# Kernel tuning notes

Measured on AMD Instinct MI355X. Metric: run time of the kernel, lower is better.

Reference implementation:

```python
import jax, jax.numpy as jnp
import numpy as np

EMBED_DIM = 1024
Q_DIM = 512
KV_DIM = 512
NUM_HEADS = 16
HEAD_DIM = EMBED_DIM // NUM_HEADS
EPS = 1e-5


def setup_inputs() -> dict:
    key = jax.random.key(0)
    ks = jax.random.split(key, 13)
    B, N1, N2 = 2, 2048, 2048
    s_q = 1.0 / np.sqrt(Q_DIM)
    s_kv = 1.0 / np.sqrt(KV_DIM)
    s_e = 1.0 / np.sqrt(EMBED_DIM)
    return {
        "query": jax.random.normal(ks[0], (B, N1, Q_DIM), jnp.float32),
        "key": jax.random.normal(ks[1], (B, N2, KV_DIM), jnp.float32),
        "value": jax.random.normal(ks[2], (B, N2, KV_DIM), jnp.float32),
        "Wq": jax.random.uniform(ks[3], (Q_DIM, EMBED_DIM), jnp.float32, -s_q, s_q),
        "bq": jax.random.uniform(ks[4], (EMBED_DIM,), jnp.float32, -s_q, s_q),
        "Wk": jax.random.uniform(ks[5], (KV_DIM, EMBED_DIM), jnp.float32, -s_kv, s_kv),
        "bk": jax.random.uniform(ks[6], (EMBED_DIM,), jnp.float32, -s_kv, s_kv),
        "Wv": jax.random.uniform(ks[7], (KV_DIM, EMBED_DIM), jnp.float32, -s_kv, s_kv),
        "bv": jax.random.uniform(ks[8], (EMBED_DIM,), jnp.float32, -s_kv, s_kv),
        "Wo": jax.random.uniform(ks[9], (EMBED_DIM, EMBED_DIM), jnp.float32, -s_e, s_e),
        "bo": jax.random.uniform(ks[10], (EMBED_DIM,), jnp.float32, -s_e, s_e),
        "gamma": jnp.ones((EMBED_DIM,), jnp.float32),
        "beta": jnp.zeros((EMBED_DIM,), jnp.float32),
    }


def reference(query, key, value, Wq, bq, Wk, bk, Wv, bv, Wo, bo, gamma, beta):
    B, N1, _ = query.shape
    _, N2, _ = key.shape
    scale = HEAD_DIM ** (-0.5)
    # projections -> [B, H, N, D]
    Q = (query @ Wq + bq).reshape(B, N1, NUM_HEADS, HEAD_DIM).transpose(0, 2, 1, 3)
    K = (key @ Wk + bk).reshape(B, N2, NUM_HEADS, HEAD_DIM).transpose(0, 2, 1, 3)
    V = (value @ Wv + bv).reshape(B, N2, NUM_HEADS, HEAD_DIM).transpose(0, 2, 1, 3)
    # full score matrix [B, H, N1, N2] (matches original eager attention)
    att = jnp.einsum("bhqd,bhkd->bhqk", Q, K) * scale
    att = jax.nn.softmax(att, axis=-1)
    # dropout is identity in eval mode
    out = jnp.einsum("bhqk,bhkd->bhqd", att, V)  # [B, H, N1, D]
    out = out.transpose(0, 2, 1, 3).reshape(B, N1, EMBED_DIM)
    out = out @ Wo + bo
    # LayerNorm
    mu = out.mean(-1, keepdims=True)
    var = ((out - mu) ** 2).mean(-1, keepdims=True)
    return (out - mu) * jax.lax.rsqrt(var + EPS) * gamma + beta
```

## Files before the change

kernel.cpp:

```cpp
#include <hip/hip_runtime.h>

typedef __bf16 bf16x8 __attribute__((ext_vector_type(8)));
typedef __bf16 bf16x4 __attribute__((ext_vector_type(4)));
typedef __bf16 bf16x2 __attribute__((ext_vector_type(2)));
typedef float f32x4 __attribute__((ext_vector_type(4)));
typedef unsigned short u16;
typedef unsigned int u32;

__device__ __forceinline__ f32x4 mfma16(bf16x8 a, bf16x8 b, f32x4 c) {
  return __builtin_amdgcn_mfma_f32_16x16x32_bf16(a, b, c, 0, 0, 0);
}

__device__ __forceinline__ void gload_lds16(const void* g, void* l) {
  __builtin_amdgcn_global_load_lds(
      (const __attribute__((address_space(1))) void*)g,
      (__attribute__((address_space(3))) void*)l, 16, 0, 0);
}

__device__ __forceinline__ void swap32(u32& a, u32& b) {
  asm volatile("v_permlane32_swap_b32 %0, %1" : "+v"(a), "+v"(b));
}
__device__ __forceinline__ void swap16(u32& a, u32& b) {
  asm volatile("v_permlane16_swap_b32 %0, %1" : "+v"(a), "+v"(b));
}

__device__ __forceinline__ u32 pkbf(float a, float b) {
  union { bf16x2 h; u32 w; } u;
  u.h[0] = (__bf16)a;
  u.h[1] = (__bf16)b;
  return u.w;
}

__global__ __launch_bounds__(256) void prep(const float4* __restrict__ qi,
                                            const float4* __restrict__ ki,
                                            const float4* __restrict__ vi,
                                            bf16x4* __restrict__ oq,
                                            bf16x4* __restrict__ ok,
                                            bf16x4* __restrict__ ov,
                                            const float* __restrict__ W0,
                                            const float* __restrict__ W1,
                                            const float* __restrict__ W2,
                                            const float* __restrict__ W3,
                                            u16* __restrict__ T0, u16* __restrict__ T1,
                                            u16* __restrict__ T2, u16* __restrict__ T3,
                                            int n4) {
  const int z = blockIdx.y;
  const int tid = threadIdx.x;
  if (z < 3) {
    int i = blockIdx.x * 256 + tid;
    if (i >= n4) return;
    const float4* in = z == 0 ? qi : z == 1 ? ki : vi;
    bf16x4* out = z == 0 ? oq : z == 1 ? ok : ov;
    float4 v = in[i];
    bf16x4 o;
    o[0] = (__bf16)v.x; o[1] = (__bf16)v.y; o[2] = (__bf16)v.z; o[3] = (__bf16)v.w;
    out[i] = o;
  } else {
    const int zz = z - 3;
    const int K = (zz == 3) ? 1024 : 512;
    const int nb = (K / 32) * 32;
    if (blockIdx.x >= nb) return;
    const float* W = zz == 0 ? W0 : zz == 1 ? W1 : zz == 2 ? W2 : W3;
    u16* Wt = zz == 0 ? T0 : zz == 1 ? T1 : zz == 2 ? T2 : T3;
    __shared__ float t[32][33];
    const int tx = tid & 31, ty = tid >> 5;
    const int n0 = (blockIdx.x & 31) * 32, k0 = (blockIdx.x >> 5) * 32;
#pragma unroll
    for (int i = 0; i < 4; ++i)
      t[ty + i * 8][tx] = W[(size_t)(k0 + ty + i * 8) * 1024 + n0 + tx];
    __syncthreads();
#pragma unroll
    for (int i = 0; i < 4; ++i)
      ((__bf16*)Wt)[(size_t)(n0 + ty + i * 8) * K + k0 + tx] = (__bf16)t[tx][ty + i * 8];
  }
}

template <int MODE, int DBUF>
__device__ __forceinline__ void gemm_body(const u16* __restrict__ A,
                                          const u16* __restrict__ Bt,
                                          const float* __restrict__ bias,
                                          void* __restrict__ Cout,
                                          int M, int N, int K, float scl) {
  constexpr int NB = DBUF ? 2 : 1;
  __shared__ __align__(16) u16 lA[NB][128 * 64];
  __shared__ __align__(16) u16 lB[NB][128 * 64];
  const int tid = threadIdx.x;
  const int w = tid >> 6, l = tid & 63;
  const int li = l & 15, lg = l >> 4;
  const int wm = w & 1, wn = w >> 1;
  const int bm = blockIdx.x * 128, bn = blockIdx.y * 128;

  f32x4 acc[4][4] = {};
  const int nk = K >> 6;

  auto stage = [&](int kt, int bufi) {
    const int k0 = kt << 6;
#pragma unroll
    for (int i = 0; i < 4; ++i) {
      const int c0 = (i * 4 + w) * 64;
      const int f = c0 + l;
      const int r = f >> 3, cs = (f & 7) ^ (r & 7);
      gload_lds16(A + (size_t)(bm + r) * K + k0 + cs * 8, &lA[bufi][c0 * 8]);
      gload_lds16(Bt + (size_t)(bn + r) * K + k0 + cs * 8, &lB[bufi][c0 * 8]);
    }
  };

  int cur = 0;
  if (DBUF) {
    stage(0, 0);
    __syncthreads();
  }

  for (int kt = 0; kt < nk; ++kt) {
    if (DBUF) {
      if (kt + 1 < nk) stage(kt + 1, cur ^ 1);
    } else {
      stage(kt, 0);
      __syncthreads();
    }
    bf16x8 af[4][2], bfr[4][2];
#pragma unroll
    for (int m = 0; m < 4; ++m) {
      const int row = wm * 64 + m * 16 + li;
#pragma unroll
      for (int kk = 0; kk < 2; ++kk) {
        const int kc = (lg + kk * 4) ^ (row & 7);
        af[m][kk] = *(const bf16x8*)&lA[cur][row * 64 + kc * 8];
      }
    }
#pragma unroll
    for (int n = 0; n < 4; ++n) {
      const int row = wn * 64 + n * 16 + li;
#pragma unroll
      for (int kk = 0; kk < 2; ++kk) {
        const int kc = (lg + kk * 4) ^ (row & 7);
        bfr[n][kk] = *(const bf16x8*)&lB[cur][row * 64 + kc * 8];
      }
    }
#pragma unroll
    for (int m = 0; m < 4; ++m)
#pragma unroll
      for (int n = 0; n < 4; ++n) {
        acc[m][n] = mfma16(af[m][0], bfr[n][0], acc[m][n]);
        acc[m][n] = mfma16(af[m][1], bfr[n][1], acc[m][n]);
      }
    __syncthreads();
    if (DBUF) cur ^= 1;
  }

#pragma unroll
  for (int m = 0; m < 4; ++m) {
    const int row0 = bm + wm * 64 + m * 16 + lg * 4;
#pragma unroll
    for (int n = 0; n < 4; ++n) {
      const int col = bn + wn * 64 + n * 16 + li;
      const float bv = bias[col];
      if (MODE == 2) {
        const int bq = row0 >> 11, kv = row0 & 2047;
        bf16x4 pk;
#pragma unroll
        for (int r = 0; r < 4; ++r) pk[r] = (__bf16)((acc[m][n][r] + bv) * scl);
        *(bf16x4*)&((u16*)Cout)[((size_t)(bq * 1024 + col)) * 2048 + kv] = pk;
      } else {
#pragma unroll
        for (int r = 0; r < 4; ++r) {
          float v = (acc[m][n][r] + bv) * scl;
          ((__bf16*)Cout)[(size_t)(row0 + r) * N + col] = (__bf16)v;
        }
      }
    }
  }
}

__global__ __launch_bounds__(256) void gemm_qkv(const u16* __restrict__ xq,
                                                const u16* __restrict__ xk,
                                                const u16* __restrict__ xv,
                                                const u16* __restrict__ wqt,
                                                const u16* __restrict__ wkt,
                                                const u16* __restrict__ wvt,
                                                const float* __restrict__ bq,
                                                const float* __restrict__ bk,
                                                const float* __restrict__ bv,
                                                u16* __restrict__ Qb, u16* __restrict__ Kb,
                                                u16* __restrict__ Vt, float qscale) {
  const int z = blockIdx.z;
  if (z == 0) {
    gemm_body<0, 0>(xq, wqt, bq, Qb, 4096, 1024, 512, qscale);
  } else if (z == 1) {
    gemm_body<0, 0>(xk, wkt, bk, Kb, 4096, 1024, 512, 1.0f);
  } else {
    gemm_body<2, 0>(xv, wvt, bv, Vt, 4096, 1024, 512, 1.0f);
  }
}

__global__ __launch_bounds__(256) void gemm_o(const u16* __restrict__ A,
                                              const u16* __restrict__ Bt,
                                              const float* __restrict__ bias,
                                              u16* __restrict__ C) {
  gemm_body<0, 1>(A, Bt, bias, C, 4096, 1024, 1024, 1.0f);
}

__global__ __launch_bounds__(512) void attn64(const u16* __restrict__ Qb,
                                              const u16* __restrict__ Kb,
                                              const u16* __restrict__ Vt,
                                              u16* __restrict__ Opart,
                                              float* __restrict__ Lpart,
                                              int N1, int N2) {
  const int tid = threadIdx.x;
  const int w = tid >> 6, l = tid & 63;
  const int li = l & 15, lg = l >> 4;

  const int flat = blockIdx.x + 8 * (blockIdx.y + 16 * blockIdx.z);
  const int xcd = flat & 7, idx = flat >> 3;
  const int qb = idx & 7, rest = idx >> 3;
  const int h = 2 * xcd + (rest & 1);
  const int b = (rest >> 1) & 1;
  const int kvh = rest >> 2;
  const int q0 = qb * 256;

  __shared__ __align__(16) u16 lK[2][64 * 64];
  __shared__ __align__(16) u16 lV[2][64 * 64];

  bf16x8 qa[2][2];
#pragma unroll
  for (int s = 0; s < 2; ++s) {
    const size_t qoff = (size_t)(b * N1 + q0 + s * 128 + w * 16 + li) * 1024 + h * 64;
    qa[s][0] = *(const bf16x8*)&Qb[qoff + lg * 8];
    qa[s][1] = *(const bf16x8*)&Qb[qoff + 32 + lg * 8];
  }

  const u16* Kbase = Kb + (size_t)b * N2 * 1024 + h * 64;
  const u16* Vbase = Vt + (size_t)((b * 16 + h) * 64) * N2;

  const int sr = tid >> 3;
  const int sc = (tid & 7) ^ (sr & 7);

  f32x4 o[2][4] = {};
  float lsum0 = 0.f, lsum1 = 0.f;
  const int ca = lg ^ (li & 7), cb = (lg + 4) ^ (li & 7);

  const int t0 = kvh * 16;
  int cur = 0;
  gload_lds16(Kbase + (size_t)(t0 * 64 + sr) * 1024 + sc * 8, &lK[0][w * 512]);
  gload_lds16(Vbase + (size_t)sr * N2 + t0 * 64 + sc * 8, &lV[0][w * 512]);
  __syncthreads();

  for (int tt = 0; tt < 16; ++tt) {
    const int t = t0 + tt;
    if (tt + 1 < 16) {
      gload_lds16(Kbase + (size_t)((t + 1) * 64 + sr) * 1024 + sc * 8, &lK[cur ^ 1][w * 512]);
      gload_lds16(Vbase + (size_t)sr * N2 + (t + 1) * 64 + sc * 8, &lV[cur ^ 1][w * 512]);
    }
    const u16* K_ = lK[cur];
    const u16* V_ = lV[cur];

    float st0 = 0.f, st1 = 0.f;
    u32 u0[4][2], u1[4][2];
    __builtin_amdgcn_s_setprio(1);
#pragma unroll
    for (int n = 0; n < 4; ++n) {
      const int row = n * 16 + li;
      bf16x8 k0 = *(const bf16x8*)&K_[row * 64 + ca * 8];
      bf16x8 k1 = *(const bf16x8*)&K_[row * 64 + cb * 8];
      f32x4 a = {}, a2 = {};
      a = mfma16(k0, qa[0][0], a);
      a = mfma16(k1, qa[0][1], a);
      a2 = mfma16(k0, qa[1][0], a2);
      a2 = mfma16(k1, qa[1][1], a2);
      float p0 = __builtin_amdgcn_exp2f(a[0]);
      float p1 = __builtin_amdgcn_exp2f(a[1]);
      float p2 = __builtin_amdgcn_exp2f(a[2]);
      float p3 = __builtin_amdgcn_exp2f(a[3]);
      st0 += (p0 + p1) + (p2 + p3);
      u0[n][0] = pkbf(p0, p1);
      u0[n][1] = pkbf(p2, p3);
      float r0 = __builtin_amdgcn_exp2f(a2[0]);
      float r1 = __builtin_amdgcn_exp2f(a2[1]);
      float r2 = __builtin_amdgcn_exp2f(a2[2]);
      float r3 = __builtin_amdgcn_exp2f(a2[3]);
      st1 += (r0 + r1) + (r2 + r3);
      u1[n][0] = pkbf(r0, r1);
      u1[n][1] = pkbf(r2, r3);
    }
    __builtin_amdgcn_s_setprio(0);
    lsum0 += st0;
    lsum1 += st1;

#pragma unroll
    for (int c = 0; c < 2; ++c) {
      swap32(u0[0][c], u0[1][c]); swap32(u0[2][c], u0[3][c]);
      swap32(u1[0][c], u1[1][c]); swap32(u1[2][c], u1[3][c]);
    }
#pragma unroll
    for (int c = 0; c < 2; ++c) {
      swap16(u0[0][c], u0[1][c]); swap16(u0[2][c], u0[3][c]);
      swap16(u1[0][c], u1[1][c]); swap16(u1[2][c], u1[3][c]);
    }

    __builtin_amdgcn_s_setprio(1);
#pragma unroll
    for (int ks = 0; ks < 2; ++ks) {
      union { u32 w4[4]; bf16x8 v; } f0, f1;
      f0.w4[0] = u0[2 * ks][0]; f0.w4[1] = u0[2 * ks][1];
      f0.w4[2] = u0[2 * ks + 1][0]; f0.w4[3] = u0[2 * ks + 1][1];
      f1.w4[0] = u1[2 * ks][0]; f1.w4[1] = u1[2 * ks][1];
      f1.w4[2] = u1[2 * ks + 1][0]; f1.w4[3] = u1[2 * ks + 1][1];
#pragma unroll
      for (int dt = 0; dt < 4; ++dt) {
        const int row = dt * 16 + li;
        const int c = (lg + ks * 4) ^ (li & 7);
        const bf16x8 vf = *(const bf16x8*)&V_[row * 64 + c * 8];
        o[0][dt] = mfma16(vf, f0.v, o[0][dt]);
        o[1][dt] = mfma16(vf, f1.v, o[1][dt]);
      }
    }
    __builtin_amdgcn_s_setprio(0);
    __syncthreads();
    cur ^= 1;
  }

  lsum0 += __shfl_xor(lsum0, 16, 64);
  lsum0 += __shfl_xor(lsum0, 32, 64);
  lsum1 += __shfl_xor(lsum1, 16, 64);
  lsum1 += __shfl_xor(lsum1, 32, 64);

  u16* Op = Opart + (size_t)kvh * 4096 * 1024;
#pragma unroll
  for (int s = 0; s < 2; ++s) {
    const int qrow = b * N1 + q0 + s * 128 + w * 16 + li;
    const size_t orow = (size_t)qrow * 1024 + h * 64;
#pragma unroll
    for (int dt = 0; dt < 4; ++dt) {
      bf16x4 pk;
#pragma unroll
      for (int r = 0; r < 4; ++r) pk[r] = (__bf16)o[s][dt][r];
      *(bf16x4*)&Op[orow + dt * 16 + lg * 4] = pk;
    }
    if (lg == 0)
      Lpart[(size_t)kvh * 4096 * 16 + (size_t)qrow * 16 + h] = (s == 0 ? lsum0 : lsum1);
  }
}

__global__ __launch_bounds__(256) void combine(const u16* __restrict__ Opart,
                                               const float* __restrict__ Lpart,
                                               u16* __restrict__ ao) {
  const int row = blockIdx.x;
  const int tid = threadIdx.x;
  const int h = tid >> 4;
  const float l = Lpart[(size_t)row * 16 + h] + Lpart[4096 * 16 + (size_t)row * 16 + h];
  const float inv = 1.f / l;
  const size_t off = (size_t)row * 1024 + tid * 4;
  const bf16x4 a = *(const bf16x4*)&Opart[off];
  const bf16x4 b = *(const bf16x4*)&Opart[(size_t)4096 * 1024 + off];
  bf16x4 o;
#pragma unroll
  for (int j = 0; j < 4; ++j) o[j] = (__bf16)(((float)a[j] + (float)b[j]) * inv);
  *(bf16x4*)&ao[off] = o;
}

__global__ __launch_bounds__(256) void lnorm(const u16* __restrict__ X,
                                             const float* __restrict__ gamma,
                                             const float* __restrict__ beta,
                                             float* __restrict__ out) {
  const int row = blockIdx.x;
  const int tid = threadIdx.x;
  const bf16x4 xv = ((const bf16x4*)(X + (size_t)row * 1024))[tid];
  float4 v;
  v.x = (float)xv[0]; v.y = (float)xv[1]; v.z = (float)xv[2]; v.w = (float)xv[3];
  float s = v.x + v.y + v.z + v.w;
  float sq = v.x * v.x + v.y * v.y + v.z * v.z + v.w * v.w;
#pragma unroll
  for (int d = 1; d < 64; d <<= 1) {
    s += __shfl_xor(s, d, 64);
    sq += __shfl_xor(sq, d, 64);
  }
  __shared__ float red[8];
  const int w = tid >> 6, l = tid & 63;
  if (l == 0) { red[w] = s; red[4 + w] = sq; }
  __syncthreads();
  s = red[0] + red[1] + red[2] + red[3];
  sq = red[4] + red[5] + red[6] + red[7];
  const float mu = s * (1.f / 1024.f);
  const float var = sq * (1.f / 1024.f) - mu * mu;
  const float rstd = rsqrtf(var + 1e-5f);
  const float4 g = ((const float4*)gamma)[tid];
  const float4 bb = ((const float4*)beta)[tid];
  float4 o;
  o.x = (v.x - mu) * rstd * g.x + bb.x;
  o.y = (v.y - mu) * rstd * g.y + bb.y;
  o.z = (v.z - mu) * rstd * g.z + bb.z;
  o.w = (v.w - mu) * rstd * g.w + bb.w;
  ((float4*)(out + (size_t)row * 1024))[tid] = o;
}

extern "C" void kernel_launch(void* const* d_in, const int* in_sizes, int n_in,
                              void* d_out, int out_size, void* d_ws, size_t ws_size,
                              hipStream_t stream) {
  const float* query = (const float*)d_in[0];
  const float* key_ = (const float*)d_in[1];
  const float* value = (const float*)d_in[2];
  const float* Wq = (const float*)d_in[3];
  const float* bq = (const float*)d_in[4];
  const float* Wk = (const float*)d_in[5];
  const float* bk = (const float*)d_in[6];
  const float* Wv = (const float*)d_in[7];
  const float* bv = (const float*)d_in[8];
  const float* Wo = (const float*)d_in[9];
  const float* bo = (const float*)d_in[10];
  const float* gamma = (const float*)d_in[11];
  const float* beta = (const float*)d_in[12];

  constexpr int B = 2, N1 = 2048, N2 = 2048, E = 1024, QKD = 512;
  constexpr int M = B * N1;
  const float QSCALE = 0.125f * 1.4426950408889634f;

  char* p = (char*)d_ws;
  auto alloc = [&](size_t bytes) {
    char* r = p;
    p += (bytes + 255) & ~(size_t)255;
    return r;
  };
  u16* xq = (u16*)alloc((size_t)M * QKD * 2);
  u16* xk = (u16*)alloc((size_t)M * QKD * 2);
  u16* xv = (u16*)alloc((size_t)M * QKD * 2);
  u16* wqt = (u16*)alloc((size_t)E * QKD * 2);
  u16* wkt = (u16*)alloc((size_t)E * QKD * 2);
  u16* wvt = (u16*)alloc((size_t)E * QKD * 2);
  u16* wot = (u16*)alloc((size_t)E * E * 2);
  u16* Qb = (u16*)alloc((size_t)M * E * 2);
  u16* Kb = (u16*)alloc((size_t)M * E * 2);
  u16* Vt = (u16*)alloc((size_t)M * E * 2);
  u16* ao = (u16*)alloc((size_t)M * E * 2);
  u16* ao2 = (u16*)alloc((size_t)M * E * 2);
  u16* Opart = (u16*)alloc((size_t)2 * M * E * 2);
  float* Lpart = (float*)alloc((size_t)2 * M * 16 * 4);

  const int n4 = M * QKD / 4;
  prep<<<dim3((n4 + 255) / 256, 7), 256, 0, stream>>>(
      (const float4*)query, (const float4*)key_, (const float4*)value,
      (bf16x4*)xq, (bf16x4*)xk, (bf16x4*)xv,
      Wq, Wk, Wv, Wo, wqt, wkt, wvt, wot, n4);

  gemm_qkv<<<dim3(M / 128, E / 128, 3), 256, 0, stream>>>(
      xq, xk, xv, wqt, wkt, wvt, bq, bk, bv, Qb, Kb, Vt, QSCALE);

  attn64<<<dim3(8, 16, 4), 512, 0, stream>>>(Qb, Kb, Vt, Opart, Lpart, N1, N2);

  combine<<<M, 256, 0, stream>>>(Opart, Lpart, ao);

  gemm_o<<<dim3(M / 128, E / 128), 256, 0, stream>>>(ao, wot, bo, ao2);

  lnorm<<<M, 256, 0, stream>>>(ao2, gamma, beta, (float*)d_out);
}
```

Baseline: 111.2 us.

## Process two KV tiles per barrier in attention and add 8-wave output GEMM

The attention kernel now uses four K/V LDS buffers and processes two 64-key tiles between barriers, prefetching two tiles ahead. This halves the number of block-wide syncs and gives more load-compute overlap, at the cost of doubling LDS use per block. A launch-bounds occupancy hint is also added. The output projection is replaced with a dedicated 512-thread GEMM kernel that uses double-buffered LDS staging and a 4x2 MFMA tile per wave, replacing the shared 256-thread gemm_body path.

New measurement: 103.6 us. 6.9% less time.

```diff
diff --git a/kernel.cpp b/kernel.cpp
--- a/kernel.cpp
+++ b/kernel.cpp
@@ -193,19 +193,90 @@
   }
 }
 
-__global__ __launch_bounds__(256) void gemm_o(const u16* __restrict__ A,
-                                              const u16* __restrict__ Bt,
-                                              const float* __restrict__ bias,
-                                              u16* __restrict__ C) {
-  gemm_body<0, 1>(A, Bt, bias, C, 4096, 1024, 1024, 1.0f);
-}
-
-__global__ __launch_bounds__(512) void attn64(const u16* __restrict__ Qb,
-                                              const u16* __restrict__ Kb,
-                                              const u16* __restrict__ Vt,
-                                              u16* __restrict__ Opart,
-                                              float* __restrict__ Lpart,
-                                              int N1, int N2) {
+__global__ __launch_bounds__(512) void gemm_o8(const u16* __restrict__ A,
+                                               const u16* __restrict__ Bt,
+                                               const float* __restrict__ bias,
+                                               u16* __restrict__ C) {
+  constexpr int N = 1024, K = 1024;
+  __shared__ __align__(16) u16 lA[2][128 * 64];
+  __shared__ __align__(16) u16 lB[2][128 * 64];
+  const int tid = threadIdx.x;
+  const int w = tid >> 6, l = tid & 63;
+  const int li = l & 15, lg = l >> 4;
+  const int wm = w & 1, wn = w >> 1;
+  const int bm = blockIdx.x * 128, bn = blockIdx.y * 128;
+
+  f32x4 acc[4][2] = {};
+  const int nk = K >> 6;
+
+  auto stage = [&](int kt, int bufi) {
+    const int k0 = kt << 6;
+#pragma unroll
+    for (int i = 0; i < 2; ++i) {
+      const int c0 = (i * 8 + w) * 64;
+      const int f = c0 + l;
+      const int r = f >> 3, cs = (f & 7) ^ (r & 7);
+      gload_lds16(A + (size_t)(bm + r) * K + k0 + cs * 8, &lA[bufi][c0 * 8]);
+      gload_lds16(Bt + (size_t)(bn + r) * K + k0 + cs * 8, &lB[bufi][c0 * 8]);
+    }
+  };
+
+  int cur = 0;
+  stage(0, 0);
+  __syncthreads();
+
+  for (int kt = 0; kt < nk; ++kt) {
+    if (kt + 1 < nk) stage(kt + 1, cur ^ 1);
+    bf16x8 af[4][2], bfr[2][2];
+#pragma unroll
+    for (int m = 0; m < 4; ++m) {
+      const int row = wm * 64 + m * 16 + li;
+#pragma unroll
+      for (int kk = 0; kk < 2; ++kk) {
+        const int kc = (lg + kk * 4) ^ (row & 7);
+        af[m][kk] = *(const bf16x8*)&lA[cur][row * 64 + kc * 8];
+      }
+    }
+#pragma unroll
+    for (int n = 0; n < 2; ++n) {
+      const int row = wn * 32 + n * 16 + li;
+#pragma unroll
+      for (int kk = 0; kk < 2; ++kk) {
+        const int kc = (lg + kk * 4) ^ (row & 7);
+        bfr[n][kk] = *(const bf16x8*)&lB[cur][row * 64 + kc * 8];
+      }
+    }
+#pragma unroll
+    for (int m = 0; m < 4; ++m)
+#pragma unroll
+      for (int n = 0; n < 2; ++n) {
+        acc[m][n] = mfma16(af[m][0], bfr[n][0], acc[m][n]);
+        acc[m][n] = mfma16(af[m][1], bfr[n][1], acc[m][n]);
+      }
+    __syncthreads();
+    cur ^= 1;
+  }
+
+#pragma unroll
+  for (int m = 0; m < 4; ++m) {
+    const int row0 = bm + wm * 64 + m * 16 + lg * 4;
+#pragma unroll
+    for (int n = 0; n < 2; ++n) {
+      const int col = bn + wn * 32 + n * 16 + li;
+      const float bv = bias[col];
+#pragma unroll
+      for (int r = 0; r < 4; ++r)
+        ((__bf16*)C)[(size_t)(row0 + r) * N + col] = (__bf16)(acc[m][n][r] + bv);
+    }
+  }
+}
+
+__global__ __launch_bounds__(512, 4) void attn64(const u16* __restrict__ Qb,
+                                                 const u16* __restrict__ Kb,
+                                                 const u16* __restrict__ Vt,
+                                                 u16* __restrict__ Opart,
+                                                 float* __restrict__ Lpart,
+                                                 int N1, int N2) {
   const int tid = threadIdx.x;
   const int w = tid >> 6, l = tid & 63;
   const int li = l & 15, lg = l >> 4;
@@ -218,8 +289,8 @@
   const int kvh = rest >> 2;
   const int q0 = qb * 256;
 
-  __shared__ __align__(16) u16 lK[2][64 * 64];
-  __shared__ __align__(16) u16 lV[2][64 * 64];
+  __shared__ __align__(16) u16 lK[4][64 * 64];
+  __shared__ __align__(16) u16 lV[4][64 * 64];
 
   bf16x8 qa[2][2];
 #pragma unroll
@@ -239,21 +310,14 @@
   float lsum0 = 0.f, lsum1 = 0.f;
   const int ca = lg ^ (li & 7), cb = (lg + 4) ^ (li & 7);
 
-  const int t0 = kvh * 16;
-  int cur = 0;
-  gload_lds16(Kbase + (size_t)(t0 * 64 + sr) * 1024 + sc * 8, &lK[0][w * 512]);
-  gload_lds16(Vbase + (size_t)sr * N2 + t0 * 64 + sc * 8, &lV[0][w * 512]);
-  __syncthreads();
-
-  for (int tt = 0; tt < 16; ++tt) {
-    const int t = t0 + tt;
-    if (tt + 1 < 16) {
-      gload_lds16(Kbase + (size_t)((t + 1) * 64 + sr) * 1024 + sc * 8, &lK[cur ^ 1][w * 512]);
-      gload_lds16(Vbase + (size_t)sr * N2 + (t + 1) * 64 + sc * 8, &lV[cur ^ 1][w * 512]);
-    }
-    const u16* K_ = lK[cur];
-    const u16* V_ = lV[cur];
-
+  auto stageK = [&](int t, int bufi) {
+    gload_lds16(Kbase + (size_t)(t * 64 + sr) * 1024 + sc * 8, &lK[bufi][w * 512]);
+  };
+  auto stageV = [&](int t, int bufi) {
+    gload_lds16(Vbase + (size_t)sr * N2 + t * 64 + sc * 8, &lV[bufi][w * 512]);
+  };
+
+  auto tile_body = [&](const u16* K_, const u16* V_) {
     float st0 = 0.f, st1 = 0.f;
     u32 u0[4][2], u1[4][2];
     __builtin_amdgcn_s_setprio(1);
@@ -315,8 +379,21 @@
       }
     }
     __builtin_amdgcn_s_setprio(0);
+  };
+
+  const int t0 = kvh * 16;
+
+  stageK(t0, 0); stageV(t0, 0);
+  stageK(t0 + 1, 1); stageV(t0 + 1, 1);
+  __syncthreads();
+
+  for (int tt = 0; tt < 16; tt += 2) {
+    const int t = t0 + tt;
+    if (tt + 2 < 16) { stageK(t + 2, (tt + 2) & 3); stageV(t + 2, (tt + 2) & 3); }
+    if (tt + 3 < 16) { stageK(t + 3, (tt + 3) & 3); stageV(t + 3, (tt + 3) & 3); }
+    tile_body(lK[tt & 3], lV[tt & 3]);
+    tile_body(lK[(tt + 1) & 3], lV[(tt + 1) & 3]);
     __syncthreads();
-    cur ^= 1;
   }
 
   lsum0 += __shfl_xor(lsum0, 16, 64);
@@ -448,7 +525,7 @@
 
   combine<<<M, 256, 0, stream>>>(Opart, Lpart, ao);
 
-  gemm_o<<<dim3(M / 128, E / 128), 256, 0, stream>>>(ao, wot, bo, ao2);
+  gemm_o8<<<dim3(M / 128, E / 128), 512, 0, stream>>>(ao, wot, bo, ao2);
 
   lnorm<<<M, 256, 0, stream>>>(ao2, gamma, beta, (float*)d_out);
 }
```
